# Optimization experiments

Measured on AMD Instinct MI355X. Metric: run time of the kernel, lower is better.

## Reference

```python
import jax, jax.numpy as jnp
import numpy as np

H, DK, DV = 8, 64, 64
BETA = 0.5
EPS = 1e-5


def _pe(length, d):
    # standard sinusoidal positional encoding, (length, d)
    pos = np.arange(length, dtype=np.float32)[:, None]
    i = np.arange(0, d, 2, dtype=np.float32)
    ang = pos / np.power(10000.0, i / d)
    pe = np.zeros((length, d), dtype=np.float32)
    pe[:, 0::2] = np.sin(ang)
    pe[:, 1::2] = np.cos(ang)
    return jnp.asarray(pe)


def _ln(x, g, b):
    m = x.mean(-1, keepdims=True)
    v = ((x - m) ** 2).mean(-1, keepdims=True)
    return (x - m) / jnp.sqrt(v + EPS) * g + b


def _mha(q_in, k_in, v_in, wq, bq, wk, bk, wv, bv, wo, bo):
    # meshed-memory style MHA; attention_mask is all-ones in this module -> no-op
    B, Sq, _ = q_in.shape
    Sk = k_in.shape[1]
    q = (q_in @ wq + bq).reshape(B, Sq, H, DK).transpose(0, 2, 1, 3)
    k = (k_in @ wk + bk).reshape(B, Sk, H, DK).transpose(0, 2, 1, 3)
    v = (v_in @ wv + bv).reshape(B, Sk, H, DV).transpose(0, 2, 1, 3)
    att = jax.nn.softmax(jnp.einsum('bhqd,bhkd->bhqk', q, k) / np.float32(np.sqrt(DK)), axis=-1)
    out = jnp.einsum('bhqk,bhkd->bhqd', att, v).transpose(0, 2, 1, 3).reshape(B, Sq, H * DV)
    return out @ wo + bo, att


def setup_inputs() -> dict:
    key = jax.random.key(0)
    ks = jax.random.split(key, 24)
    d, n_e = 512, 64
    B, S_enc, T = 16, 1024, 2048
    s = 0.02
    inp = {
        'x_enc': jax.random.normal(ks[0], (B, S_enc, d), jnp.float32),
        'z': jax.random.normal(ks[1], (B, T, d), jnp.float32),
        'emb_table': jax.random.normal(ks[2], (n_e, d), jnp.float32),
    }
    names = ['sha_wq', 'sha_wk', 'sha_wv', 'sha_wo', 'esha_wq', 'esha_wk', 'esha_wv', 'esha_wo']
    for i, n in enumerate(names):
        inp[n] = jax.random.normal(ks[3 + i], (d, d), jnp.float32) * s
        inp[n.replace('w', 'b')] = jnp.zeros((d,), jnp.float32)
    inp['esha_ln_g'] = jnp.ones((d,), jnp.float32)
    inp['esha_ln_b'] = jnp.zeros((d,), jnp.float32)
    inp['norm_g'] = jnp.ones((d,), jnp.float32)
    inp['norm_b'] = jnp.zeros((d,), jnp.float32)
    return inp


def reference(x_enc, z, emb_table, sha_wq, sha_bq, sha_wk, sha_bk, sha_wv, sha_bv, sha_wo, sha_bo,
              esha_wq, esha_bq, esha_wk, esha_bk, esha_wv, esha_bv, esha_wo, esha_bo,
              esha_ln_g, esha_ln_b, norm_g, norm_b):
    B = x_enc.shape[0]
    n_e, d = emb_table.shape
    # --- create_conditioned_embedding ---
    emb = jnp.broadcast_to(emb_table[None], (B, n_e, d)) + _pe(n_e, d)[None]
    y, _ = _mha(emb, x_enc, x_enc, sha_wq, sha_bq, sha_wk, sha_bk, sha_wv, sha_bv, sha_wo, sha_bo)
    emb = _ln(emb + y, norm_g, norm_b)
    y2, _ = _mha(emb, emb, emb, esha_wq, esha_bq, esha_wk, esha_bk, esha_wv, esha_bv, esha_wo, esha_bo)
    emb = _ln(emb + y2, esha_ln_g, esha_ln_b)  # proj = Identity (d_proj == d_model)
    # --- vqvae_min_encodings: squared distances (B, T, n_e) ---
    d2 = ((z * z).sum(-1)[:, :, None] + (emb * emb).sum(-1)[:, None, :]
          - 2.0 * jnp.einsum('btd,bkd->btk', z, emb))
    idx = jnp.argmin(d2, axis=-1)                      # (B, T)
    enc = jax.nn.one_hot(idx, n_e, dtype=z.dtype)      # (B, T, n_e)
    # --- extract_zq: one-hot gather via matmul ---
    z_q = jnp.einsum('btk,bkd->btd', enc, emb)
    sg = jax.lax.stop_gradient
    loss = (BETA * jnp.mean((sg(z_q) - z) ** 2) + jnp.mean((z_q - sg(z)) ** 2)).reshape(1)
    z_q = z + sg(z_q - z)  # straight-through
    e_mean = enc.reshape(-1, n_e).mean(0)
    perplexity = jnp.exp(-jnp.sum(e_mean * jnp.log(e_mean + 1e-10)))
    return z_q, loss, perplexity, enc.reshape(-1, n_e), idx, emb
```

## Files before the change

kernel.cpp:

```cpp
#include <hip/hip_runtime.h>
#include <math.h>

#define DD     512
#define NBATCH 16
#define SENC   1024
#define TTOK   2048
#define NHEAD  8
#define HDIM   64
#define NE     64

#define WS_K1    0
#define WS_V1    (WS_K1 + NBATCH*SENC*DD)
#define WS_EMB0  (WS_V1 + NBATCH*SENC*DD)
#define WS_Q1    (WS_EMB0 + NE*DD)
#define WS_ATT1  (WS_Q1 + NE*DD)
#define WS_EMB1  (WS_ATT1 + NBATCH*NE*DD)
#define WS_Q2    (WS_EMB1 + NBATCH*NE*DD)
#define WS_K2    (WS_Q2 + NBATCH*NE*DD)
#define WS_V2    (WS_K2 + NBATCH*NE*DD)
#define WS_ATT2  (WS_V2 + NBATCH*NE*DD)
#define WS_YBUF  (WS_ATT2 + NBATCH*NE*DD)
#define WS_EMBF  (WS_YBUF + NBATCH*NE*DD)
#define WS_E2    (WS_EMBF + NBATCH*NE*DD)
#define WS_LOSSP (WS_E2 + 2*NBATCH*NE)
#define WS_CNT   (WS_LOSSP + 2*512)

#define OUT_ZQ   0
#define OUT_LOSS (NBATCH*TTOK*DD)
#define OUT_PERP (OUT_LOSS + 1)
#define OUT_ENC  (OUT_PERP + 1)
#define OUT_IDX  (OUT_ENC + NBATCH*TTOK*NE)
#define OUT_EMB  (OUT_IDX + NBATCH*TTOK)

__global__ __launch_bounds__(256) void pe_emb0_k(const float* __restrict__ tab,
                                                 float* __restrict__ emb0)
{
    int p = blockIdx.x;
    for (int c = threadIdx.x; c < DD; c += 256) {
        int ie = c & ~1;
        float denom = (float)pow(10000.0, (double)ie / 512.0);
        float ang = (float)p / denom;
        double v = (c & 1) ? cos((double)ang) : sin((double)ang);
        emb0[p * DD + c] = tab[p * DD + c] + (float)v;
    }
}

__global__ __launch_bounds__(256) void gemm_kv_k(
    const float* __restrict__ A,
    const float* __restrict__ W0, const float* __restrict__ B0, float* __restrict__ C0,
    const float* __restrict__ W1, const float* __restrict__ B1, float* __restrict__ C1)
{
    __shared__ float As[32][132];
    __shared__ float Ws[2][32][68];
    const int n0 = blockIdx.x * 64;
    const int m0 = blockIdx.y * 128;
    const int tid = threadIdx.x;
    const int tx = tid & 15, ty = tid >> 4;

    float acc[2][8][4];
#pragma unroll
    for (int o = 0; o < 2; ++o)
#pragma unroll
        for (int i = 0; i < 8; ++i)
#pragma unroll
            for (int j = 0; j < 4; ++j) acc[o][i][j] = 0.f;

    const float* Wp[2] = {W0, W1};

    for (int kk = 0; kk < DD; kk += 32) {
        __syncthreads();
#pragma unroll
        for (int l = 0; l < 4; ++l) {
            int fid = l * 256 + tid;
            int row = fid >> 3, c4 = fid & 7;
            float4 v = *reinterpret_cast<const float4*>(&A[(size_t)(m0 + row) * DD + kk + c4 * 4]);
            As[c4 * 4 + 0][row] = v.x;
            As[c4 * 4 + 1][row] = v.y;
            As[c4 * 4 + 2][row] = v.z;
            As[c4 * 4 + 3][row] = v.w;
        }
#pragma unroll
        for (int o = 0; o < 2; ++o) {
#pragma unroll
            for (int l = 0; l < 2; ++l) {
                int fid = l * 256 + tid;
                int kr = fid >> 4, c4 = fid & 15;
                *reinterpret_cast<float4*>(&Ws[o][kr][c4 * 4]) =
                    *reinterpret_cast<const float4*>(&Wp[o][(size_t)(kk + kr) * DD + n0 + c4 * 4]);
            }
        }
        __syncthreads();
#pragma unroll 8
        for (int k = 0; k < 32; ++k) {
            float4 a0 = *reinterpret_cast<const float4*>(&As[k][ty * 8]);
            float4 a1 = *reinterpret_cast<const float4*>(&As[k][ty * 8 + 4]);
            float a[8] = {a0.x, a0.y, a0.z, a0.w, a1.x, a1.y, a1.z, a1.w};
#pragma unroll
            for (int o = 0; o < 2; ++o) {
                float4 wv = *reinterpret_cast<const float4*>(&Ws[o][k][tx * 4]);
#pragma unroll
                for (int i = 0; i < 8; ++i) {
                    acc[o][i][0] = fmaf(a[i], wv.x, acc[o][i][0]);
                    acc[o][i][1] = fmaf(a[i], wv.y, acc[o][i][1]);
                    acc[o][i][2] = fmaf(a[i], wv.z, acc[o][i][2]);
                    acc[o][i][3] = fmaf(a[i], wv.w, acc[o][i][3]);
                }
            }
        }
    }
    float* Cp[2] = {C0, C1};
    const float* Bp[2] = {B0, B1};
#pragma unroll
    for (int o = 0; o < 2; ++o) {
        float4 bv = *reinterpret_cast<const float4*>(&Bp[o][n0 + tx * 4]);
#pragma unroll
        for (int i = 0; i < 8; ++i) {
            int row = m0 + ty * 8 + i;
            float4 o4 = {acc[o][i][0] + bv.x, acc[o][i][1] + bv.y,
                         acc[o][i][2] + bv.z, acc[o][i][3] + bv.w};
            *reinterpret_cast<float4*>(&Cp[o][(size_t)row * DD + n0 + tx * 4]) = o4;
        }
    }
}

template <int NOUT>
__global__ __launch_bounds__(256) void gemm_bias_k(
    const float* __restrict__ A,
    const float* __restrict__ W0, const float* __restrict__ B0, float* __restrict__ C0,
    const float* __restrict__ W1, const float* __restrict__ B1, float* __restrict__ C1,
    const float* __restrict__ W2, const float* __restrict__ B2, float* __restrict__ C2)
{
    __shared__ float As[32][64];
    __shared__ float Ws[NOUT][32][64];
    const int m0 = blockIdx.x * 64;
    const int n0 = blockIdx.y * 64;
    const int tid = threadIdx.x;
    const int tx = tid & 15, ty = tid >> 4;

    float acc[NOUT][4][4];
#pragma unroll
    for (int o = 0; o < NOUT; ++o)
#pragma unroll
        for (int i = 0; i < 4; ++i)
#pragma unroll
            for (int j = 0; j < 4; ++j) acc[o][i][j] = 0.f;

    const float* Wp[3] = {W0, W1, W2};

    for (int kk = 0; kk < DD; kk += 32) {
        __syncthreads();
#pragma unroll
        for (int l = 0; l < 2; ++l) {
            int fid = l * 256 + tid;
            int row = fid >> 3, c4 = fid & 7;
            float4 v = *reinterpret_cast<const float4*>(&A[(size_t)(m0 + row) * DD + kk + c4 * 4]);
            As[c4 * 4 + 0][row] = v.x;
            As[c4 * 4 + 1][row] = v.y;
            As[c4 * 4 + 2][row] = v.z;
            As[c4 * 4 + 3][row] = v.w;
        }
#pragma unroll
        for (int o = 0; o < NOUT; ++o) {
#pragma unroll
            for (int l = 0; l < 2; ++l) {
                int fid = l * 256 + tid;
                int kr = fid >> 4, c4 = fid & 15;
                *reinterpret_cast<float4*>(&Ws[o][kr][c4 * 4]) =
                    *reinterpret_cast<const float4*>(&Wp[o][(size_t)(kk + kr) * DD + n0 + c4 * 4]);
            }
        }
        __syncthreads();
#pragma unroll
        for (int k = 0; k < 32; ++k) {
            float4 av = *reinterpret_cast<const float4*>(&As[k][ty * 4]);
            float a[4] = {av.x, av.y, av.z, av.w};
#pragma unroll
            for (int o = 0; o < NOUT; ++o) {
                float4 wv = *reinterpret_cast<const float4*>(&Ws[o][k][tx * 4]);
#pragma unroll
                for (int i = 0; i < 4; ++i) {
                    acc[o][i][0] = fmaf(a[i], wv.x, acc[o][i][0]);
                    acc[o][i][1] = fmaf(a[i], wv.y, acc[o][i][1]);
                    acc[o][i][2] = fmaf(a[i], wv.z, acc[o][i][2]);
                    acc[o][i][3] = fmaf(a[i], wv.w, acc[o][i][3]);
                }
            }
        }
    }
    float* Cp[3] = {C0, C1, C2};
    const float* Bp[3] = {B0, B1, B2};
#pragma unroll
    for (int o = 0; o < NOUT; ++o) {
#pragma unroll
        for (int i = 0; i < 4; ++i) {
            int row = m0 + ty * 4 + i;
#pragma unroll
            for (int j = 0; j < 4; ++j) {
                int col = n0 + tx * 4 + j;
                Cp[o][(size_t)row * DD + col] = acc[o][i][j] + Bp[o][col];
            }
        }
    }
}

__global__ __launch_bounds__(256) void attn_k(
    const float* __restrict__ q, int q_shared,
    const float* __restrict__ kmat, const float* __restrict__ vmat,
    float* __restrict__ outp, int slen)
{
    __shared__ float qs[64][68];
    __shared__ float kst[64][68];
    __shared__ float vs[64][68];
    int b = blockIdx.x >> 3, h = blockIdx.x & 7;
    int tid = threadIdx.x;
    const float* qb = q + (q_shared ? (size_t)0 : (size_t)b * 64 * DD);
    const float* kb = kmat + (size_t)b * slen * DD;
    const float* vb = vmat + (size_t)b * slen * DD;

#pragma unroll
    for (int l = 0; l < 4; ++l) {
        int fid = l * 256 + tid;
        int r = fid >> 4, c4 = fid & 15;
        *reinterpret_cast<float4*>(&qs[r][c4 * 4]) =
            *reinterpret_cast<const float4*>(&qb[(size_t)r * DD + h * HDIM + c4 * 4]);
    }
    const int row = tid >> 2, c4 = tid & 3;
    float acc[16];
#pragma unroll
    for (int i = 0; i < 16; ++i) acc[i] = 0.f;
    float m_run = -INFINITY, l_run = 0.f;

    for (int s0 = 0; s0 < slen; s0 += 64) {
        __syncthreads();
#pragma unroll
        for (int l = 0; l < 4; ++l) {
            int fid = l * 256 + tid;
            int r = fid >> 4, cc = fid & 15;
            float4 t4 = *reinterpret_cast<const float4*>(&kb[(size_t)(s0 + r) * DD + h * HDIM + cc * 4]);
            kst[cc * 4 + 0][r] = t4.x;
            kst[cc * 4 + 1][r] = t4.y;
            kst[cc * 4 + 2][r] = t4.z;
            kst[cc * 4 + 3][r] = t4.w;
            *reinterpret_cast<float4*>(&vs[r][cc * 4]) =
                *reinterpret_cast<const float4*>(&vb[(size_t)(s0 + r) * DD + h * HDIM + cc * 4]);
        }
        __syncthreads();

        float p[16];
#pragma unroll
        for (int i = 0; i < 16; ++i) p[i] = 0.f;
#pragma unroll 4
        for (int e = 0; e < 64; ++e) {
            float qv = qs[row][e];
#pragma unroll
            for (int j4 = 0; j4 < 4; ++j4) {
                float4 k4 = *reinterpret_cast<const float4*>(&kst[e][c4 * 16 + j4 * 4]);
                p[j4 * 4 + 0] = fmaf(qv, k4.x, p[j4 * 4 + 0]);
                p[j4 * 4 + 1] = fmaf(qv, k4.y, p[j4 * 4 + 1]);
                p[j4 * 4 + 2] = fmaf(qv, k4.z, p[j4 * 4 + 2]);
                p[j4 * 4 + 3] = fmaf(qv, k4.w, p[j4 * 4 + 3]);
            }
        }
#pragma unroll
        for (int i = 0; i < 16; ++i) p[i] *= 0.125f;
        float mx = p[0];
#pragma unroll
        for (int i = 1; i < 16; ++i) mx = fmaxf(mx, p[i]);
        mx = fmaxf(mx, __shfl_xor(mx, 1));
        mx = fmaxf(mx, __shfl_xor(mx, 2));
        float m_new = fmaxf(m_run, mx);
        float scale = expf(m_run - m_new);
        float lsum = 0.f;
#pragma unroll
        for (int i = 0; i < 16; ++i) { p[i] = expf(p[i] - m_new); lsum += p[i]; }
        lsum += __shfl_xor(lsum, 1);
        lsum += __shfl_xor(lsum, 2);
        l_run = l_run * scale + lsum;
        m_run = m_new;
#pragma unroll
        for (int i = 0; i < 16; ++i) acc[i] *= scale;

#pragma unroll 16
        for (int j = 0; j < 64; ++j) {
            float pv = __shfl(p[j & 15], j >> 4, 4);
#pragma unroll
            for (int u = 0; u < 4; ++u) {
                float4 v4 = *reinterpret_cast<const float4*>(&vs[j][c4 * 16 + u * 4]);
                acc[u * 4 + 0] = fmaf(pv, v4.x, acc[u * 4 + 0]);
                acc[u * 4 + 1] = fmaf(pv, v4.y, acc[u * 4 + 1]);
                acc[u * 4 + 2] = fmaf(pv, v4.z, acc[u * 4 + 2]);
                acc[u * 4 + 3] = fmaf(pv, v4.w, acc[u * 4 + 3]);
            }
        }
    }
#pragma unroll
    for (int i = 0; i < 16; ++i) acc[i] /= l_run;
#pragma unroll
    for (int u = 0; u < 4; ++u) {
        float4 o4 = {acc[u * 4 + 0], acc[u * 4 + 1], acc[u * 4 + 2], acc[u * 4 + 3]};
        *reinterpret_cast<float4*>(&outp[((size_t)b * 64 + row) * DD + h * HDIM + c4 * 16 + u * 4]) = o4;
    }
}

__device__ __forceinline__ float block_sum256(float v, float* sb)
{
#pragma unroll
    for (int off = 32; off; off >>= 1) v += __shfl_down(v, off);
    __syncthreads();
    if ((threadIdx.x & 63) == 0) sb[threadIdx.x >> 6] = v;
    __syncthreads();
    return (sb[0] + sb[1]) + (sb[2] + sb[3]);
}

__global__ __launch_bounds__(256) void ln_k(
    const float* __restrict__ res, int res_shared, const float* __restrict__ y,
    const float* __restrict__ g, const float* __restrict__ bb,
    float* __restrict__ out, float* __restrict__ out2, double* __restrict__ e2)
{
    __shared__ float sbuf[4];
    __shared__ double dbuf[4];
    int row = blockIdx.x;
    int t = threadIdx.x;
    const float* rp = res + (size_t)(res_shared ? (row & 63) : row) * DD;
    const float* yp = y + (size_t)row * DD;
    float x0 = rp[t] + yp[t];
    float x1 = rp[t + 256] + yp[t + 256];
    float m = block_sum256(x0 + x1, sbuf) / 512.0f;
    float d0 = x0 - m, d1 = x1 - m;
    float v = block_sum256(d0 * d0 + d1 * d1, sbuf) / 512.0f;
    float s = sqrtf(v + 1e-5f);
    float o0 = d0 / s * g[t] + bb[t];
    float o1 = d1 / s * g[t + 256] + bb[t + 256];
    out[(size_t)row * DD + t] = o0;
    out[(size_t)row * DD + t + 256] = o1;
    if (out2) {
        out2[(size_t)row * DD + t] = o0;
        out2[(size_t)row * DD + t + 256] = o1;
    }
    if (e2) {
        double sd = (double)o0 * o0 + (double)o1 * o1;
#pragma unroll
        for (int off = 32; off; off >>= 1) sd += __shfl_down(sd, off);
        if ((t & 63) == 0) dbuf[t >> 6] = sd;
        __syncthreads();
        if (t == 0) e2[row] = (dbuf[0] + dbuf[1]) + (dbuf[2] + dbuf[3]);
    }
}

__global__ __launch_bounds__(512) void vq_k(
    const float* __restrict__ z, const float* __restrict__ emb,
    const double* __restrict__ e2,
    float* __restrict__ zq, float* __restrict__ enc, float* __restrict__ idxo,
    double* __restrict__ lossp, int* __restrict__ counts)
{
    __shared__ float zs[32][68];
    __shared__ float es[32][68];
    __shared__ int   kms[64];
    __shared__ double dred[8];
    __shared__ int   cnt_s[64];

    const int bid = blockIdx.x;
    const int b   = bid >> 5;
    const int m0  = (bid & 31) * 64;
    const int tid = threadIdx.x;
    const int tx  = tid & 15, ty = tid >> 4;

    const float* zb = z   + ((size_t)b * TTOK + m0) * DD;
    const float* eb = emb + (size_t)b * NE * DD;

    double acc[2][4];
#pragma unroll
    for (int r = 0; r < 2; ++r)
#pragma unroll
        for (int j = 0; j < 4; ++j) acc[r][j] = 0.0;

    const int lrow = tid >> 3, lc4 = tid & 7;

    for (int kk = 0; kk < DD; kk += 32) {
        __syncthreads();
        {
            float4 t4 = *reinterpret_cast<const float4*>(&zb[(size_t)lrow * DD + kk + lc4 * 4]);
            zs[lc4 * 4 + 0][lrow] = t4.x;
            zs[lc4 * 4 + 1][lrow] = t4.y;
            zs[lc4 * 4 + 2][lrow] = t4.z;
            zs[lc4 * 4 + 3][lrow] = t4.w;
            float4 e4 = *reinterpret_cast<const float4*>(&eb[(size_t)lrow * DD + kk + lc4 * 4]);
            es[lc4 * 4 + 0][lrow] = e4.x;
            es[lc4 * 4 + 1][lrow] = e4.y;
            es[lc4 * 4 + 2][lrow] = e4.z;
            es[lc4 * 4 + 3][lrow] = e4.w;
        }
        __syncthreads();
#pragma unroll
        for (int k = 0; k < 32; ++k) {
            float2 zv = *reinterpret_cast<const float2*>(&zs[k][ty * 2]);
            float4 ev = *reinterpret_cast<const float4*>(&es[k][tx * 4]);
            double z0 = (double)zv.x, z1 = (double)zv.y;
            double e0 = (double)ev.x, e1 = (double)ev.y;
            double e2d = (double)ev.z, e3 = (double)ev.w;
            acc[0][0] = fma(z0, e0, acc[0][0]);
            acc[0][1] = fma(z0, e1, acc[0][1]);
            acc[0][2] = fma(z0, e2d, acc[0][2]);
            acc[0][3] = fma(z0, e3, acc[0][3]);
            acc[1][0] = fma(z1, e0, acc[1][0]);
            acc[1][1] = fma(z1, e1, acc[1][1]);
            acc[1][2] = fma(z1, e2d, acc[1][2]);
            acc[1][3] = fma(z1, e3, acc[1][3]);
        }
    }

    double e2v[4];
#pragma unroll
    for (int j = 0; j < 4; ++j) e2v[j] = e2[b * NE + tx * 4 + j];

    double vmin[2]; int imin[2];
#pragma unroll
    for (int r = 0; r < 2; ++r) {
        vmin[r] = e2v[0] - 2.0 * acc[r][0];
        imin[r] = tx * 4;
#pragma unroll
        for (int j = 1; j < 4; ++j) {
            double s = e2v[j] - 2.0 * acc[r][j];
            if (s < vmin[r]) { vmin[r] = s; imin[r] = tx * 4 + j; }
        }
    }
#pragma unroll
    for (int off = 1; off < 16; off <<= 1) {
#pragma unroll
        for (int r = 0; r < 2; ++r) {
            double ov = __shfl_xor(vmin[r], off);
            int    oi = __shfl_xor(imin[r], off);
            if (ov < vmin[r] || (ov == vmin[r] && oi < imin[r])) { vmin[r] = ov; imin[r] = oi; }
        }
    }
    if (tid < 64) cnt_s[tid] = 0;
    if (tx == 0) { kms[ty * 2] = imin[0]; kms[ty * 2 + 1] = imin[1]; }
    __syncthreads();
    if (tid < 64) atomicAdd(&cnt_s[kms[tid]], 1);

    const int row = tid >> 3, p = tid & 7;
    const int km  = kms[row];
    const float* zr = &zb[(size_t)row * DD];
    const float* er = &eb[(size_t)km * DD];
    const size_t grow = (size_t)b * TTOK + m0 + row;
    float* zqr = zq + grow * DD;
    double lsum = 0.0;
#pragma unroll 4
    for (int i = 0; i < 16; ++i) {
        int col = (i * 8 + p) * 4;
        float4 zv = *reinterpret_cast<const float4*>(&zr[col]);
        float4 ev = *reinterpret_cast<const float4*>(&er[col]);
        float d0 = ev.x - zv.x, d1 = ev.y - zv.y, d2 = ev.z - zv.z, d3 = ev.w - zv.w;
        lsum += (double)d0 * d0 + (double)d1 * d1 + (double)d2 * d2 + (double)d3 * d3;
        float4 o4 = {zv.x + d0, zv.y + d1, zv.z + d2, zv.w + d3};
        *reinterpret_cast<float4*>(&zqr[col]) = o4;
    }
    {
        float* ep = enc + grow * NE + p * 8;
        float4 o0, o1;
        o0.x = (p * 8 + 0 == km) ? 1.f : 0.f;
        o0.y = (p * 8 + 1 == km) ? 1.f : 0.f;
        o0.z = (p * 8 + 2 == km) ? 1.f : 0.f;
        o0.w = (p * 8 + 3 == km) ? 1.f : 0.f;
        o1.x = (p * 8 + 4 == km) ? 1.f : 0.f;
        o1.y = (p * 8 + 5 == km) ? 1.f : 0.f;
        o1.z = (p * 8 + 6 == km) ? 1.f : 0.f;
        o1.w = (p * 8 + 7 == km) ? 1.f : 0.f;
        *reinterpret_cast<float4*>(ep)     = o0;
        *reinterpret_cast<float4*>(ep + 4) = o1;
    }
    if (tid < 64) idxo[(size_t)b * TTOK + m0 + tid] = (float)kms[tid];

#pragma unroll
    for (int off = 32; off; off >>= 1) lsum += __shfl_down(lsum, off);
    if ((tid & 63) == 0) dred[tid >> 6] = lsum;
    __syncthreads();
    if (tid == 0) {
        double t = 0.0;
#pragma unroll
        for (int w = 0; w < 8; ++w) t += dred[w];
        lossp[bid] = t;
    }
    if (tid < 64 && cnt_s[tid]) atomicAdd(&counts[tid], cnt_s[tid]);
}

__global__ void fin_k(const double* __restrict__ lossp, const int* __restrict__ counts,
                      float* __restrict__ loss_out, float* __restrict__ perp_out)
{
    int tid = threadIdx.x;
    if (tid == 0) {
        double tot = 0.0;
        for (int i = 0; i < 512; ++i) tot += lossp[i];
        loss_out[0] = (float)(1.5 * tot / 16777216.0);
    }
    float e = counts[tid] / 32768.0f;
    float term = e * logf(e + 1e-10f);
#pragma unroll
    for (int off = 32; off; off >>= 1) term += __shfl_down(term, off);
    if (tid == 0) perp_out[0] = expf(-term);
}

extern "C" void kernel_launch(void* const* d_in, const int* in_sizes, int n_in,
                              void* d_out, int out_size, void* d_ws, size_t ws_size,
                              hipStream_t stream)
{
    (void)in_sizes; (void)n_in; (void)out_size; (void)ws_size;
    const float* x_enc = (const float*)d_in[0];
    const float* z     = (const float*)d_in[1];
    const float* tab   = (const float*)d_in[2];
    const float* wq1 = (const float*)d_in[3];  const float* bq1 = (const float*)d_in[4];
    const float* wk1 = (const float*)d_in[5];  const float* bk1 = (const float*)d_in[6];
    const float* wv1 = (const float*)d_in[7];  const float* bv1 = (const float*)d_in[8];
    const float* wo1 = (const float*)d_in[9];  const float* bo1 = (const float*)d_in[10];
    const float* wq2 = (const float*)d_in[11]; const float* bq2 = (const float*)d_in[12];
    const float* wk2 = (const float*)d_in[13]; const float* bk2 = (const float*)d_in[14];
    const float* wv2 = (const float*)d_in[15]; const float* bv2 = (const float*)d_in[16];
    const float* wo2 = (const float*)d_in[17]; const float* bo2 = (const float*)d_in[18];
    const float* ln2g = (const float*)d_in[19]; const float* ln2b = (const float*)d_in[20];
    const float* ln1g = (const float*)d_in[21]; const float* ln1b = (const float*)d_in[22];

    float* ws  = (float*)d_ws;
    float* out = (float*)d_out;

    float* k1   = ws + WS_K1;
    float* v1   = ws + WS_V1;
    float* emb0 = ws + WS_EMB0;
    float* q1   = ws + WS_Q1;
    float* att1 = ws + WS_ATT1;
    float* emb1 = ws + WS_EMB1;
    float* q2   = ws + WS_Q2;
    float* k2   = ws + WS_K2;
    float* v2   = ws + WS_V2;
    float* att2 = ws + WS_ATT2;
    float* ybuf = ws + WS_YBUF;
    float* embf = ws + WS_EMBF;
    double* e2    = (double*)(ws + WS_E2);
    double* lossp = (double*)(ws + WS_LOSSP);
    int*    cnts  = (int*)(ws + WS_CNT);

    hipMemsetAsync(cnts, 0, NE * sizeof(int), stream);

    pe_emb0_k<<<64, 256, 0, stream>>>(tab, emb0);

    gemm_bias_k<1><<<dim3(1, 8), 256, 0, stream>>>(emb0, wq1, bq1, q1,
                                                   nullptr, nullptr, nullptr,
                                                   nullptr, nullptr, nullptr);
    gemm_kv_k<<<dim3(8, 128), 256, 0, stream>>>(x_enc, wk1, bk1, k1,
                                                wv1, bv1, v1);
    attn_k<<<128, 256, 0, stream>>>(q1, 1, k1, v1, att1, SENC);

    gemm_bias_k<1><<<dim3(16, 8), 256, 0, stream>>>(att1, wo1, bo1, ybuf,
                                                    nullptr, nullptr, nullptr,
                                                    nullptr, nullptr, nullptr);
    ln_k<<<1024, 256, 0, stream>>>(emb0, 1, ybuf, ln1g, ln1b, emb1, nullptr, nullptr);

    gemm_bias_k<3><<<dim3(16, 8), 256, 0, stream>>>(emb1, wq2, bq2, q2,
                                                    wk2, bk2, k2,
                                                    wv2, bv2, v2);
    attn_k<<<128, 256, 0, stream>>>(q2, 0, k2, v2, att2, 64);

    gemm_bias_k<1><<<dim3(16, 8), 256, 0, stream>>>(att2, wo2, bo2, ybuf,
                                                    nullptr, nullptr, nullptr,
                                                    nullptr, nullptr, nullptr);
    ln_k<<<1024, 256, 0, stream>>>(emb1, 0, ybuf, ln2g, ln2b, embf, out + OUT_EMB, e2);

    vq_k<<<512, 512, 0, stream>>>(z, embf, e2,
                                  out + OUT_ZQ, out + OUT_ENC, out + OUT_IDX,
                                  lossp, cnts);
    fin_k<<<1, 64, 0, stream>>>(lossp, cnts, out + OUT_LOSS, out + OUT_PERP);
}
```

Baseline: 611.7 us.

## Prefetch next K-tile into registers and remap KV GEMM blocks per XCD

The KV projection GEMM now loads the next 32-wide K slice of A and both weight matrices into registers while the current shared-memory tile is being consumed. This hides global-load latency behind the FMA loop. The grid is also flattened to 1D and remapped so that blocks landing on the same XCD (round-robin by block id) share the same A row-tiles, which improves L2 reuse of x_enc. The cost is more live registers, which may reduce occupancy.

New measurement: 605.6 us. Within noise of the previous version (-1.0%).

```diff
diff --git a/kernel.cpp b/kernel.cpp
--- a/kernel.cpp
+++ b/kernel.cpp
@@ -52,11 +52,17 @@
 {
     __shared__ float As[32][132];
     __shared__ float Ws[2][32][68];
-    const int n0 = blockIdx.x * 64;
-    const int m0 = blockIdx.y * 128;
+    const int bid = blockIdx.x;
+    const int xcd = bid & 7;
+    const int idx = bid >> 3;
+    const int m0 = (xcd * 16 + (idx >> 3)) * 128;
+    const int n0 = (idx & 7) * 64;
     const int tid = threadIdx.x;
     const int tx = tid & 15, ty = tid >> 4;
 
+    const int ar = tid >> 3, ac4 = tid & 7;
+    const int wr = tid >> 4, wc4 = tid & 15;
+
     float acc[2][8][4];
 #pragma unroll
     for (int o = 0; o < 2; ++o)
@@ -65,49 +71,74 @@
 #pragma unroll
             for (int j = 0; j < 4; ++j) acc[o][i][j] = 0.f;
 
-    const float* Wp[2] = {W0, W1};
-
-    for (int kk = 0; kk < DD; kk += 32) {
-        __syncthreads();
-#pragma unroll
-        for (int l = 0; l < 4; ++l) {
-            int fid = l * 256 + tid;
-            int row = fid >> 3, c4 = fid & 7;
-            float4 v = *reinterpret_cast<const float4*>(&A[(size_t)(m0 + row) * DD + kk + c4 * 4]);
-            As[c4 * 4 + 0][row] = v.x;
-            As[c4 * 4 + 1][row] = v.y;
-            As[c4 * 4 + 2][row] = v.z;
-            As[c4 * 4 + 3][row] = v.w;
-        }
-#pragma unroll
-        for (int o = 0; o < 2; ++o) {
-#pragma unroll
-            for (int l = 0; l < 2; ++l) {
-                int fid = l * 256 + tid;
-                int kr = fid >> 4, c4 = fid & 15;
-                *reinterpret_cast<float4*>(&Ws[o][kr][c4 * 4]) =
-                    *reinterpret_cast<const float4*>(&Wp[o][(size_t)(kk + kr) * DD + n0 + c4 * 4]);
-            }
-        }
-        __syncthreads();
+    float4 ra0, ra1, ra2, ra3;
+    float4 rw00, rw01, rw10, rw11;
+
+#define LOADS(KK)                                                                         \
+    ra0 = *reinterpret_cast<const float4*>(&A[(size_t)(m0 + ar +  0) * DD + (KK) + ac4 * 4]); \
+    ra1 = *reinterpret_cast<const float4*>(&A[(size_t)(m0 + ar + 32) * DD + (KK) + ac4 * 4]); \
+    ra2 = *reinterpret_cast<const float4*>(&A[(size_t)(m0 + ar + 64) * DD + (KK) + ac4 * 4]); \
+    ra3 = *reinterpret_cast<const float4*>(&A[(size_t)(m0 + ar + 96) * DD + (KK) + ac4 * 4]); \
+    rw00 = *reinterpret_cast<const float4*>(&W0[(size_t)((KK) + wr +  0) * DD + n0 + wc4 * 4]); \
+    rw01 = *reinterpret_cast<const float4*>(&W0[(size_t)((KK) + wr + 16) * DD + n0 + wc4 * 4]); \
+    rw10 = *reinterpret_cast<const float4*>(&W1[(size_t)((KK) + wr +  0) * DD + n0 + wc4 * 4]); \
+    rw11 = *reinterpret_cast<const float4*>(&W1[(size_t)((KK) + wr + 16) * DD + n0 + wc4 * 4]);
+
+#define STORES()                                                                          \
+    As[ac4 * 4 + 0][ar +  0] = ra0.x; As[ac4 * 4 + 1][ar +  0] = ra0.y;                   \
+    As[ac4 * 4 + 2][ar +  0] = ra0.z; As[ac4 * 4 + 3][ar +  0] = ra0.w;                   \
+    As[ac4 * 4 + 0][ar + 32] = ra1.x; As[ac4 * 4 + 1][ar + 32] = ra1.y;                   \
+    As[ac4 * 4 + 2][ar + 32] = ra1.z; As[ac4 * 4 + 3][ar + 32] = ra1.w;                   \
+    As[ac4 * 4 + 0][ar + 64] = ra2.x; As[ac4 * 4 + 1][ar + 64] = ra2.y;                   \
+    As[ac4 * 4 + 2][ar + 64] = ra2.z; As[ac4 * 4 + 3][ar + 64] = ra2.w;                   \
+    As[ac4 * 4 + 0][ar + 96] = ra3.x; As[ac4 * 4 + 1][ar + 96] = ra3.y;                   \
+    As[ac4 * 4 + 2][ar + 96] = ra3.z; As[ac4 * 4 + 3][ar + 96] = ra3.w;                   \
+    *reinterpret_cast<float4*>(&Ws[0][wr +  0][wc4 * 4]) = rw00;                          \
+    *reinterpret_cast<float4*>(&Ws[0][wr + 16][wc4 * 4]) = rw01;                          \
+    *reinterpret_cast<float4*>(&Ws[1][wr +  0][wc4 * 4]) = rw10;                          \
+    *reinterpret_cast<float4*>(&Ws[1][wr + 16][wc4 * 4]) = rw11;
+
+    LOADS(0)
+    STORES()
+    __syncthreads();
+
+    for (int t = 0; t < 16; ++t) {
+        if (t < 15) { LOADS((t + 1) * 32) }
 #pragma unroll 8
         for (int k = 0; k < 32; ++k) {
             float4 a0 = *reinterpret_cast<const float4*>(&As[k][ty * 8]);
             float4 a1 = *reinterpret_cast<const float4*>(&As[k][ty * 8 + 4]);
             float a[8] = {a0.x, a0.y, a0.z, a0.w, a1.x, a1.y, a1.z, a1.w};
-#pragma unroll
-            for (int o = 0; o < 2; ++o) {
-                float4 wv = *reinterpret_cast<const float4*>(&Ws[o][k][tx * 4]);
+            {
+                float4 wv = *reinterpret_cast<const float4*>(&Ws[0][k][tx * 4]);
 #pragma unroll
                 for (int i = 0; i < 8; ++i) {
-                    acc[o][i][0] = fmaf(a[i], wv.x, acc[o][i][0]);
-                    acc[o][i][1] = fmaf(a[i], wv.y, acc[o][i][1]);
-                    acc[o][i][2] = fmaf(a[i], wv.z, acc[o][i][2]);
-                    acc[o][i][3] = fmaf(a[i], wv.w, acc[o][i][3]);
+                    acc[0][i][0] = fmaf(a[i], wv.x, acc[0][i][0]);
+                    acc[0][i][1] = fmaf(a[i], wv.y, acc[0][i][1]);
+                    acc[0][i][2] = fmaf(a[i], wv.z, acc[0][i][2]);
+                    acc[0][i][3] = fmaf(a[i], wv.w, acc[0][i][3]);
                 }
             }
-        }
-    }
+            {
+                float4 wv = *reinterpret_cast<const float4*>(&Ws[1][k][tx * 4]);
+#pragma unroll
+                for (int i = 0; i < 8; ++i) {
+                    acc[1][i][0] = fmaf(a[i], wv.x, acc[1][i][0]);
+                    acc[1][i][1] = fmaf(a[i], wv.y, acc[1][i][1]);
+                    acc[1][i][2] = fmaf(a[i], wv.z, acc[1][i][2]);
+                    acc[1][i][3] = fmaf(a[i], wv.w, acc[1][i][3]);
+                }
+            }
+        }
+        __syncthreads();
+        if (t < 15) {
+            STORES()
+            __syncthreads();
+        }
+    }
+#undef LOADS
+#undef STORES
+
     float* Cp[2] = {C0, C1};
     const float* Bp[2] = {B0, B1};
 #pragma unroll
@@ -545,8 +576,8 @@
     gemm_bias_k<1><<<dim3(1, 8), 256, 0, stream>>>(emb0, wq1, bq1, q1,
                                                    nullptr, nullptr, nullptr,
                                                    nullptr, nullptr, nullptr);
-    gemm_kv_k<<<dim3(8, 128), 256, 0, stream>>>(x_enc, wk1, bk1, k1,
-                                                wv1, bv1, v1);
+    gemm_kv_k<<<1024, 256, 0, stream>>>(x_enc, wk1, bk1, k1,
+                                        wv1, bv1, v1);
     attn_k<<<128, 256, 0, stream>>>(q1, 1, k1, v1, att1, SENC);
 
     gemm_bias_k<1><<<dim3(16, 8), 256, 0, stream>>>(att1, wo1, bo1, ybuf,
```

## Enlarge K/V projection tiles with XCD-aware block mapping and split attention rows

Applied to the files above, without the earlier changes.

The fused K/V projection GEMM now gives each block a 256-row tile instead of 128, with 16 accumulator rows per thread, so each weight tile loaded is reused across more rows. A 1D grid is remapped so that blocks landing on the same XCD work on neighbouring row ranges, which should improve L2 locality. The attention kernel splits the 64 query rows into two halves across blocks of 128 threads, doubling the block count for better CU occupancy, at the cost of loading K/V twice. The larger GEMM tile raises register pressure and may reduce occupancy.

New measurement: 582.0 us. 4.9% less time.

```diff
diff --git a/kernel.cpp b/kernel.cpp
--- a/kernel.cpp
+++ b/kernel.cpp
@@ -50,27 +50,28 @@
     const float* __restrict__ W0, const float* __restrict__ B0, float* __restrict__ C0,
     const float* __restrict__ W1, const float* __restrict__ B1, float* __restrict__ C1)
 {
-    __shared__ float As[32][132];
+    __shared__ float As[32][260];
     __shared__ float Ws[2][32][68];
-    const int n0 = blockIdx.x * 64;
-    const int m0 = blockIdx.y * 128;
+    const int bid = blockIdx.x;
+    const int xcd = bid & 7;
+    const int idx = bid >> 3;
+    const int m0 = (xcd * 8 + (idx >> 3)) * 256;
+    const int n0 = (idx & 7) * 64;
     const int tid = threadIdx.x;
     const int tx = tid & 15, ty = tid >> 4;
 
-    float acc[2][8][4];
+    float acc[2][16][4];
 #pragma unroll
     for (int o = 0; o < 2; ++o)
 #pragma unroll
-        for (int i = 0; i < 8; ++i)
+        for (int i = 0; i < 16; ++i)
 #pragma unroll
             for (int j = 0; j < 4; ++j) acc[o][i][j] = 0.f;
 
-    const float* Wp[2] = {W0, W1};
-
     for (int kk = 0; kk < DD; kk += 32) {
         __syncthreads();
 #pragma unroll
-        for (int l = 0; l < 4; ++l) {
+        for (int l = 0; l < 8; ++l) {
             int fid = l * 256 + tid;
             int row = fid >> 3, c4 = fid & 7;
             float4 v = *reinterpret_cast<const float4*>(&A[(size_t)(m0 + row) * DD + kk + c4 * 4]);
@@ -79,32 +80,38 @@
             As[c4 * 4 + 2][row] = v.z;
             As[c4 * 4 + 3][row] = v.w;
         }
-#pragma unroll
-        for (int o = 0; o < 2; ++o) {
-#pragma unroll
-            for (int l = 0; l < 2; ++l) {
-                int fid = l * 256 + tid;
-                int kr = fid >> 4, c4 = fid & 15;
-                *reinterpret_cast<float4*>(&Ws[o][kr][c4 * 4]) =
-                    *reinterpret_cast<const float4*>(&Wp[o][(size_t)(kk + kr) * DD + n0 + c4 * 4]);
-            }
-        }
-        __syncthreads();
-#pragma unroll 8
+        {
+            int kr = tid >> 4, c4 = tid & 15;
+            *reinterpret_cast<float4*>(&Ws[0][kr][c4 * 4]) =
+                *reinterpret_cast<const float4*>(&W0[(size_t)(kk + kr) * DD + n0 + c4 * 4]);
+            *reinterpret_cast<float4*>(&Ws[0][kr + 16][c4 * 4]) =
+                *reinterpret_cast<const float4*>(&W0[(size_t)(kk + kr + 16) * DD + n0 + c4 * 4]);
+            *reinterpret_cast<float4*>(&Ws[1][kr][c4 * 4]) =
+                *reinterpret_cast<const float4*>(&W1[(size_t)(kk + kr) * DD + n0 + c4 * 4]);
+            *reinterpret_cast<float4*>(&Ws[1][kr + 16][c4 * 4]) =
+                *reinterpret_cast<const float4*>(&W1[(size_t)(kk + kr + 16) * DD + n0 + c4 * 4]);
+        }
+        __syncthreads();
+#pragma unroll 4
         for (int k = 0; k < 32; ++k) {
-            float4 a0 = *reinterpret_cast<const float4*>(&As[k][ty * 8]);
-            float4 a1 = *reinterpret_cast<const float4*>(&As[k][ty * 8 + 4]);
-            float a[8] = {a0.x, a0.y, a0.z, a0.w, a1.x, a1.y, a1.z, a1.w};
-#pragma unroll
-            for (int o = 0; o < 2; ++o) {
-                float4 wv = *reinterpret_cast<const float4*>(&Ws[o][k][tx * 4]);
-#pragma unroll
-                for (int i = 0; i < 8; ++i) {
-                    acc[o][i][0] = fmaf(a[i], wv.x, acc[o][i][0]);
-                    acc[o][i][1] = fmaf(a[i], wv.y, acc[o][i][1]);
-                    acc[o][i][2] = fmaf(a[i], wv.z, acc[o][i][2]);
-                    acc[o][i][3] = fmaf(a[i], wv.w, acc[o][i][3]);
-                }
+            float4 a0 = *reinterpret_cast<const float4*>(&As[k][ty * 16]);
+            float4 a1 = *reinterpret_cast<const float4*>(&As[k][ty * 16 + 4]);
+            float4 a2 = *reinterpret_cast<const float4*>(&As[k][ty * 16 + 8]);
+            float4 a3 = *reinterpret_cast<const float4*>(&As[k][ty * 16 + 12]);
+            float a[16] = {a0.x, a0.y, a0.z, a0.w, a1.x, a1.y, a1.z, a1.w,
+                           a2.x, a2.y, a2.z, a2.w, a3.x, a3.y, a3.z, a3.w};
+            float4 w0 = *reinterpret_cast<const float4*>(&Ws[0][k][tx * 4]);
+            float4 w1 = *reinterpret_cast<const float4*>(&Ws[1][k][tx * 4]);
+#pragma unroll
+            for (int i = 0; i < 16; ++i) {
+                acc[0][i][0] = fmaf(a[i], w0.x, acc[0][i][0]);
+                acc[0][i][1] = fmaf(a[i], w0.y, acc[0][i][1]);
+                acc[0][i][2] = fmaf(a[i], w0.z, acc[0][i][2]);
+                acc[0][i][3] = fmaf(a[i], w0.w, acc[0][i][3]);
+                acc[1][i][0] = fmaf(a[i], w1.x, acc[1][i][0]);
+                acc[1][i][1] = fmaf(a[i], w1.y, acc[1][i][1]);
+                acc[1][i][2] = fmaf(a[i], w1.z, acc[1][i][2]);
+                acc[1][i][3] = fmaf(a[i], w1.w, acc[1][i][3]);
             }
         }
     }
@@ -114,8 +121,8 @@
     for (int o = 0; o < 2; ++o) {
         float4 bv = *reinterpret_cast<const float4*>(&Bp[o][n0 + tx * 4]);
 #pragma unroll
-        for (int i = 0; i < 8; ++i) {
-            int row = m0 + ty * 8 + i;
+        for (int i = 0; i < 16; ++i) {
+            int row = m0 + ty * 16 + i;
             float4 o4 = {acc[o][i][0] + bv.x, acc[o][i][1] + bv.y,
                          acc[o][i][2] + bv.z, acc[o][i][3] + bv.w};
             *reinterpret_cast<float4*>(&Cp[o][(size_t)row * DD + n0 + tx * 4]) = o4;
@@ -203,15 +210,16 @@
     }
 }
 
-__global__ __launch_bounds__(256) void attn_k(
+__global__ __launch_bounds__(128) void attn_k(
     const float* __restrict__ q, int q_shared,
     const float* __restrict__ kmat, const float* __restrict__ vmat,
     float* __restrict__ outp, int slen)
 {
-    __shared__ float qs[64][68];
+    __shared__ float qs[32][68];
     __shared__ float kst[64][68];
     __shared__ float vs[64][68];
-    int b = blockIdx.x >> 3, h = blockIdx.x & 7;
+    int bid = blockIdx.x;
+    int b = bid >> 4, h = (bid >> 1) & 7, half = bid & 1;
     int tid = threadIdx.x;
     const float* qb = q + (q_shared ? (size_t)0 : (size_t)b * 64 * DD);
     const float* kb = kmat + (size_t)b * slen * DD;
@@ -219,10 +227,10 @@
 
 #pragma unroll
     for (int l = 0; l < 4; ++l) {
-        int fid = l * 256 + tid;
+        int fid = l * 128 + tid;
         int r = fid >> 4, c4 = fid & 15;
         *reinterpret_cast<float4*>(&qs[r][c4 * 4]) =
-            *reinterpret_cast<const float4*>(&qb[(size_t)r * DD + h * HDIM + c4 * 4]);
+            *reinterpret_cast<const float4*>(&qb[(size_t)(half * 32 + r) * DD + h * HDIM + c4 * 4]);
     }
     const int row = tid >> 2, c4 = tid & 3;
     float acc[16];
@@ -233,8 +241,8 @@
     for (int s0 = 0; s0 < slen; s0 += 64) {
         __syncthreads();
 #pragma unroll
-        for (int l = 0; l < 4; ++l) {
-            int fid = l * 256 + tid;
+        for (int l = 0; l < 8; ++l) {
+            int fid = l * 128 + tid;
             int r = fid >> 4, cc = fid & 15;
             float4 t4 = *reinterpret_cast<const float4*>(&kb[(size_t)(s0 + r) * DD + h * HDIM + cc * 4]);
             kst[cc * 4 + 0][r] = t4.x;
@@ -298,7 +306,7 @@
 #pragma unroll
     for (int u = 0; u < 4; ++u) {
         float4 o4 = {acc[u * 4 + 0], acc[u * 4 + 1], acc[u * 4 + 2], acc[u * 4 + 3]};
-        *reinterpret_cast<float4*>(&outp[((size_t)b * 64 + row) * DD + h * HDIM + c4 * 16 + u * 4]) = o4;
+        *reinterpret_cast<float4*>(&outp[((size_t)b * 64 + half * 32 + row) * DD + h * HDIM + c4 * 16 + u * 4]) = o4;
     }
 }
 
@@ -545,9 +553,9 @@
     gemm_bias_k<1><<<dim3(1, 8), 256, 0, stream>>>(emb0, wq1, bq1, q1,
                                                    nullptr, nullptr, nullptr,
                                                    nullptr, nullptr, nullptr);
-    gemm_kv_k<<<dim3(8, 128), 256, 0, stream>>>(x_enc, wk1, bk1, k1,
-                                                wv1, bv1, v1);
-    attn_k<<<128, 256, 0, stream>>>(q1, 1, k1, v1, att1, SENC);
+    gemm_kv_k<<<512, 256, 0, stream>>>(x_enc, wk1, bk1, k1,
+                                       wv1, bv1, v1);
+    attn_k<<<256, 128, 0, stream>>>(q1, 1, k1, v1, att1, SENC);
 
     gemm_bias_k<1><<<dim3(16, 8), 256, 0, stream>>>(att1, wo1, bo1, ybuf,
                                                     nullptr, nullptr, nullptr,
@@ -557,7 +565,7 @@
     gemm_bias_k<3><<<dim3(16, 8), 256, 0, stream>>>(emb1, wq2, bq2, q2,
                                                     wk2, bk2, k2,
                                                     wv2, bv2, v2);
-    attn_k<<<128, 256, 0, stream>>>(q2, 0, k2, v2, att2, 64);
+    attn_k<<<256, 128, 0, stream>>>(q2, 0, k2, v2, att2, 64);
 
     gemm_bias_k<1><<<dim3(16, 8), 256, 0, stream>>>(att2, wo2, bo2, ybuf,
                                                     nullptr, nullptr, nullptr,
```
